# Optimization experiments

Measured on AMD Instinct MI355X. Metric: run time of the kernel, lower is better.

Reference implementation:

```python
import jax, jax.numpy as jnp
import numpy as np

B, S, E = 8, 2048, 512

def setup_inputs() -> dict:
    key = jax.random.key(0)
    ks = jax.random.split(key, 7)
    Q = jax.random.normal(ks[0], (B, S, E), dtype=jnp.float32)
    K = jax.random.normal(ks[1], (B, S, E), dtype=jnp.float32)
    pad_mask = jax.random.randint(ks[2], (B, S, S), 0, 2).astype(bool)
    # torch nn.Linear weights are [out, in]; y = x @ W.T + b
    sc = 1.0 / np.sqrt(E)
    Wq = jax.random.uniform(ks[3], (E, E), jnp.float32, -sc, sc)
    Wk = jax.random.uniform(ks[4], (E, E), jnp.float32, -sc, sc)
    Wv = jax.random.uniform(ks[5], (E, E), jnp.float32, -sc, sc)
    Wp = jax.random.uniform(ks[6], (E, E), jnp.float32, -sc, sc)
    bp = jnp.zeros((E,), jnp.float32)
    return {"Q": Q, "K": K, "pad_mask": pad_mask, "Wq": Wq, "Wk": Wk, "Wv": Wv, "Wp": Wp, "bp": bp}

def reference(Q, K, pad_mask, Wq, Wk, Wv, Wp, bp):
    scale = E ** (-0.5)
    V = K  # V aliases K before projection, as in the original
    q = jnp.einsum('bse,fe->bsf', Q, Wq)   # q_map (no bias)
    k = jnp.einsum('bse,fe->bsf', K, Wk)   # k_map
    v = jnp.einsum('bse,fe->bsf', V, Wv)   # v_map
    scores = jnp.einsum('bqe,bke->bqk', q, k) * scale  # [B,S,S]
    scores = jnp.where(pad_mask, -1e9, scores)
    attn = jax.nn.softmax(scores, axis=-1)
    out = jnp.einsum('bqk,bke->bqe', attn, v)
    out = jnp.einsum('bse,fe->bsf', out, Wp) + bp       # proj
    return q + out  # residual uses projected Q (faithful to source)
```

## Files before the change

### kernel.cpp

```cpp
#include <hip/hip_runtime.h>
#include <hip/hip_bf16.h>

typedef short v8s __attribute__((ext_vector_type(8)));
typedef float v4f __attribute__((ext_vector_type(4)));

static constexpr int BB = 8, SS = 2048, EE = 512;

enum { EPI_BF16 = 0, EPI_SCALE = 1, EPI_FINAL = 2 };

struct EpiParams {
  float scale;
  const float* bias;
  const __hip_bfloat16* resid;
  int resid_ld;
};

static constexpr int SMEM_BYTES = 34816;

struct CastParams {
  const float* src[4];
  __hip_bfloat16* dst[4];
};

__global__ __launch_bounds__(256) void cast_weights(CastParams cp) {
  const int seg = blockIdx.x >> 7;
  const int b = blockIdx.x & 127;
  const float* x = cp.src[seg] + (unsigned long long)b * 2048;
  __hip_bfloat16* y = cp.dst[seg] + (unsigned long long)b * 2048;
  int i = threadIdx.x * 8;
  float4 f0 = ((const float4*)(x + i))[0];
  float4 f1 = ((const float4*)(x + i))[1];
  alignas(16) __hip_bfloat16 h[8];
  h[0] = __float2bfloat16(f0.x); h[1] = __float2bfloat16(f0.y);
  h[2] = __float2bfloat16(f0.z); h[3] = __float2bfloat16(f0.w);
  h[4] = __float2bfloat16(f1.x); h[5] = __float2bfloat16(f1.y);
  h[6] = __float2bfloat16(f1.z); h[7] = __float2bfloat16(f1.w);
  *(uint4*)(y + i) = *(uint4*)h;
}

__device__ __forceinline__ void stage_tile64(const __hip_bfloat16* __restrict__ G,
                                             int row0, int ld, int k0,
                                             __hip_bfloat16* lds, int wave, int lane) {
#pragma unroll
  for (int t = 0; t < 4; ++t) {
    const int p = (wave * 4 + t) * 64 + lane;
    const int row = p >> 3;
    const int g = (p & 7) ^ (row & 7);
    const __hip_bfloat16* src = G + (unsigned long long)(row0 + row) * ld + k0 + g * 8;
    __builtin_amdgcn_global_load_lds(
        (const __attribute__((address_space(1))) void*)src,
        (__attribute__((address_space(3))) void*)(lds + (wave * 4 + t) * 512),
        16, 0, 0);
  }
}

__device__ __forceinline__ void stage_tile64_f32(const float* __restrict__ G,
                                                 int row0, int ld, int k0,
                                                 __hip_bfloat16* lds, int tid) {
#pragma unroll
  for (int c = 0; c < 4; ++c) {
    const int p = c * 256 + tid;
    const int row = p >> 3;
    const int g = (p & 7) ^ (row & 7);
    const float* src = G + (unsigned long long)(row0 + row) * ld + k0 + g * 8;
    float4 f0 = ((const float4*)src)[0];
    float4 f1 = ((const float4*)src)[1];
    alignas(16) __hip_bfloat16 h[8];
    h[0] = __float2bfloat16(f0.x); h[1] = __float2bfloat16(f0.y);
    h[2] = __float2bfloat16(f0.z); h[3] = __float2bfloat16(f0.w);
    h[4] = __float2bfloat16(f1.x); h[5] = __float2bfloat16(f1.y);
    h[6] = __float2bfloat16(f1.z); h[7] = __float2bfloat16(f1.w);
    *(uint4*)&lds[p * 8] = *(uint4*)h;
  }
}

template <int EPI, bool AF32, bool BF32>
__device__ __forceinline__ void gemm_body(const void* Agv, const void* Bgv,
                                          void* Cg, int K, int lda, int ldb, int ldc,
                                          int m0, int n0, const EpiParams& ep,
                                          unsigned char* smem) {
  __hip_bfloat16* As = (__hip_bfloat16*)smem;
  __hip_bfloat16* Bs = As + 128 * 64;

  const int tid = threadIdx.x;
  const int lane = tid & 63;
  const int wave = tid >> 6;
  const int wr = wave >> 1;
  const int wc = wave & 1;

  v4f acc[4][4];
  const v4f vzero = {0.f, 0.f, 0.f, 0.f};
#pragma unroll
  for (int i = 0; i < 4; ++i)
#pragma unroll
    for (int j = 0; j < 4; ++j) acc[i][j] = vzero;

  const int fr = lane & 15;
  const int fq = lane >> 4;

  for (int k0 = 0; k0 < K; k0 += 64) {
    __syncthreads();
    if constexpr (AF32)
      stage_tile64_f32((const float*)Agv, m0, lda, k0, As, tid);
    else
      stage_tile64((const __hip_bfloat16*)Agv, m0, lda, k0, As, wave, lane);
    if constexpr (BF32)
      stage_tile64_f32((const float*)Bgv, n0, ldb, k0, Bs, tid);
    else
      stage_tile64((const __hip_bfloat16*)Bgv, n0, ldb, k0, Bs, wave, lane);
    __syncthreads();

#pragma unroll
    for (int ks = 0; ks < 2; ++ks) {
      const int gq = ks * 4 + fq;
      v8s a[4], b[4];
#pragma unroll
      for (int i = 0; i < 4; ++i) {
        const int r = wr * 64 + i * 16 + fr;
        a[i] = *(const v8s*)&As[r * 64 + ((gq ^ (r & 7)) * 8)];
      }
#pragma unroll
      for (int j = 0; j < 4; ++j) {
        const int r = wc * 64 + j * 16 + fr;
        b[j] = *(const v8s*)&Bs[r * 64 + ((gq ^ (r & 7)) * 8)];
      }
#pragma unroll
      for (int i = 0; i < 4; ++i)
#pragma unroll
        for (int j = 0; j < 4; ++j)
          acc[i][j] = __builtin_amdgcn_mfma_f32_16x16x32_bf16(a[i], b[j], acc[i][j], 0, 0, 0);
    }
  }

  const int cf = lane & 15;
  const int rq = (lane >> 4) * 4;

  __syncthreads();

  if constexpr (EPI != EPI_FINAL) {
    __hip_bfloat16* Ct = (__hip_bfloat16*)smem;
    const int ST = 136;
#pragma unroll
    for (int i = 0; i < 4; ++i) {
      const int rl = wr * 64 + i * 16 + rq;
#pragma unroll
      for (int j = 0; j < 4; ++j) {
        const int col = wc * 64 + j * 16 + cf;
#pragma unroll
        for (int r = 0; r < 4; ++r) {
          float v = acc[i][j][r];
          if constexpr (EPI == EPI_SCALE) v *= ep.scale;
          Ct[(rl + r) * ST + col] = __float2bfloat16(v);
        }
      }
    }
    __syncthreads();
    __hip_bfloat16* C = (__hip_bfloat16*)Cg;
#pragma unroll
    for (int c = 0; c < 8; ++c) {
      const int idx = c * 256 + tid;
      const int row = idx >> 4;
      const int colc = (idx & 15) * 8;
      *(v8s*)&C[(unsigned long long)(m0 + row) * ldc + n0 + colc] =
          *(const v8s*)&Ct[row * ST + colc];
    }
  } else {
    float* Cf = (float*)smem;
    const int ST = 132;
    float* C = (float*)Cg;
#pragma unroll
    for (int h = 0; h < 2; ++h) {
      if (wr == h) {
#pragma unroll
        for (int i = 0; i < 4; ++i) {
          const int rl = i * 16 + rq;
#pragma unroll
          for (int j = 0; j < 4; ++j) {
            const int col = wc * 64 + j * 16 + cf;
#pragma unroll
            for (int r = 0; r < 4; ++r) Cf[(rl + r) * ST + col] = acc[i][j][r];
          }
        }
      }
      __syncthreads();
#pragma unroll
      for (int c = 0; c < 8; ++c) {
        const int idx = c * 256 + tid;
        const int row = idx >> 5;
        const int colc = (idx & 31) * 4;
        const int grow = m0 + h * 64 + row;
        const int gcol = n0 + colc;
        float4 v = *(const float4*)&Cf[row * ST + colc];
        float4 b4 = *(const float4*)&ep.bias[gcol];
        ushort4 r4 = *(const ushort4*)&ep.resid[(unsigned long long)grow * ep.resid_ld + gcol];
        v.x += b4.x + __bfloat162float(*(__hip_bfloat16*)&r4.x);
        v.y += b4.y + __bfloat162float(*(__hip_bfloat16*)&r4.y);
        v.z += b4.z + __bfloat162float(*(__hip_bfloat16*)&r4.z);
        v.w += b4.w + __bfloat162float(*(__hip_bfloat16*)&r4.w);
        *(float4*)&C[(unsigned long long)grow * ldc + gcol] = v;
      }
      if (h == 0) __syncthreads();
    }
  }
}

template <int EPI>
__global__ __launch_bounds__(256, 3) void gemm_bt(
    const __hip_bfloat16* __restrict__ Ag, const __hip_bfloat16* __restrict__ Bg,
    void* __restrict__ Cg, int K, int lda, int ldb, int ldc,
    unsigned long long sAz, unsigned long long sBz, unsigned long long sCz, EpiParams ep) {
  __shared__ __align__(16) unsigned char smem[SMEM_BYTES];
  const unsigned long long z = blockIdx.z;
  void* Cz;
  if constexpr (EPI == EPI_FINAL) Cz = (void*)((float*)Cg + z * sCz);
  else Cz = (void*)((__hip_bfloat16*)Cg + z * sCz);
  gemm_body<EPI, false, false>(Ag + z * sAz, Bg + z * sBz, Cz, K, lda, ldb, ldc,
                               blockIdx.y * 128, blockIdx.x * 128, ep, smem);
}

__global__ __launch_bounds__(256, 3) void gemm_qkv(
    const float* __restrict__ Q, const float* __restrict__ K,
    const __hip_bfloat16* __restrict__ Wq, const __hip_bfloat16* __restrict__ Wk,
    const __hip_bfloat16* __restrict__ Wv,
    __hip_bfloat16* __restrict__ qb, __hip_bfloat16* __restrict__ kb,
    __hip_bfloat16* __restrict__ vT) {
  __shared__ __align__(16) unsigned char smem[SMEM_BYTES];
  const int z = blockIdx.z;
  EpiParams ep{};
  if (z == 2) {
    gemm_body<EPI_BF16, false, true>(Wv, K, vT, EE, EE, EE, BB * SS,
                                     blockIdx.y * 128, blockIdx.x * 128, ep, smem);
  } else {
    const float* A = (z == 0) ? Q : K;
    const __hip_bfloat16* B = (z == 0) ? Wq : Wk;
    __hip_bfloat16* C = (z == 0) ? qb : kb;
    gemm_body<EPI_BF16, true, false>(A, B, C, EE, EE, EE, EE,
                                     blockIdx.x * 128, blockIdx.y * 128, ep, smem);
  }
}

static constexpr int FLASH_LDS = 149248;

__device__ __forceinline__ void stage_K64(const __hip_bfloat16* __restrict__ Kb, int kv0,
                                          __hip_bfloat16* lds, int tid) {
  const int wv = tid >> 6;
#pragma unroll
  for (int c = 0; c < 8; ++c) {
    const int p = c * 512 + tid;
    const int chunk = p >> 9;
    const int row = (p >> 3) & 63;
    const int g = (p & 7) ^ (row & 7);
    const __hip_bfloat16* src = Kb + (unsigned long long)(kv0 + row) * 512ull + chunk * 64 + g * 8;
    __builtin_amdgcn_global_load_lds(
        (const __attribute__((address_space(1))) void*)src,
        (__attribute__((address_space(3))) void*)(lds + (c * 512 + wv * 64) * 8),
        16, 0, 0);
  }
}

__device__ __forceinline__ void stage_mask(const unsigned char* __restrict__ Mb, int kv0,
                                           unsigned char* lds, int tid) {
  if (tid < 256) {
    const int row = tid >> 2;
    const int g = tid & 3;
    const unsigned char* src = Mb + (unsigned long long)row * 2048ull + kv0 + g * 16;
    __builtin_amdgcn_global_load_lds(
        (const __attribute__((address_space(1))) void*)src,
        (__attribute__((address_space(3))) void*)(lds + tid * 16),
        16, 0, 0);
  }
}

__global__ __launch_bounds__(512, 2) void flash_attn(
    const __hip_bfloat16* __restrict__ qb, const __hip_bfloat16* __restrict__ kb,
    const __hip_bfloat16* __restrict__ vT, const unsigned char* __restrict__ mask,
    __hip_bfloat16* __restrict__ ob) {
  extern __shared__ __align__(16) char fsm[];
  __hip_bfloat16* Ks0 = (__hip_bfloat16*)fsm;
  __hip_bfloat16* Ps  = (__hip_bfloat16*)(fsm + 131072);
  unsigned char* Msk  = (unsigned char*)(fsm + 139264);
  float* m_s  = (float*)(fsm + 147456);
  float* l_s  = (float*)(fsm + 147968);
  float* pmax = (float*)(fsm + 148224);
  float* psum = (float*)(fsm + 148736);

  const int tid = threadIdx.x;
  const int lane = tid & 63;
  const int w = tid >> 6;
  const int fr = lane & 15;
  const int fq = lane >> 4;
  const int wq = w & 3;
  const int wk = w >> 2;
  const int b = blockIdx.x & 7;
  const int q0 = (blockIdx.x >> 3) * 64;
  const unsigned long long bS = (unsigned long long)b * 2048ull;
  const float SC = 0.044194173824159216f;

  v8s qf[16];
  {
    const __hip_bfloat16* qrow = qb + (bS + q0 + wq * 16 + fr) * 512ull;
#pragma unroll
    for (int kk = 0; kk < 16; ++kk) qf[kk] = *(const v8s*)&qrow[kk * 32 + fq * 8];
  }

  v4f acc[4][4];
  const v4f vz = {0.f, 0.f, 0.f, 0.f};
#pragma unroll
  for (int i = 0; i < 4; ++i)
#pragma unroll
    for (int j = 0; j < 4; ++j) acc[i][j] = vz;

  if (tid < 64) { m_s[tid] = -1e30f; l_s[tid] = 0.f; }

  const __hip_bfloat16* Kb = kb + bS * 512ull;
  const unsigned char* Mb = mask + (bS + q0) * 2048ull;
  stage_K64(Kb, 0, Ks0, tid);
  stage_mask(Mb, 0, Msk, tid);
  __syncthreads();

  for (int t = 0; t < 32; ++t) {
    __hip_bfloat16* KsT = Ks0 + (t & 1) * 32768;
    const unsigned char* mskT = Msk + (t & 1) * 4096;
    const int kv0 = t * 64;

    if (t < 31) {
      stage_K64(Kb, (t + 1) * 64, Ks0 + ((t + 1) & 1) * 32768, tid);
      stage_mask(Mb, (t + 1) * 64, Msk + ((t + 1) & 1) * 4096, tid);
    }

    v8s vb[2][4];
#pragma unroll
    for (int ks = 0; ks < 2; ++ks)
#pragma unroll
      for (int j = 0; j < 4; ++j)
        vb[ks][j] = *(const v8s*)&vT[(unsigned long long)(w * 64 + j * 16 + fr) * 16384ull +
                                     bS + kv0 + ks * 32 + fq * 8];

    v4f sa[2] = {vz, vz};
    __builtin_amdgcn_s_setprio(1);
#pragma unroll
    for (int kk = 0; kk < 16; ++kk) {
#pragma unroll
      for (int j = 0; j < 2; ++j) {
        const int rr = wk * 32 + j * 16 + fr;
        v8s kf = *(const v8s*)&KsT[(kk >> 1) * 4096 + rr * 64 + ((((kk & 1) * 4 + fq) ^ (rr & 7)) * 8)];
        sa[j] = __builtin_amdgcn_mfma_f32_16x16x32_bf16(qf[kk], kf, sa[j], 0, 0, 0);
      }
    }
    __builtin_amdgcn_s_setprio(0);

    float sv[2][4];
    float rmx[4] = {-3e38f, -3e38f, -3e38f, -3e38f};
#pragma unroll
    for (int j = 0; j < 2; ++j) {
      const int col = wk * 32 + j * 16 + fr;
#pragma unroll
      for (int r = 0; r < 4; ++r) {
        const unsigned char mk = mskT[(wq * 16 + fq * 4 + r) * 64 + col];
        const float x = mk ? -1e9f : sa[j][r] * SC;
        sv[j][r] = x;
        rmx[r] = fmaxf(rmx[r], x);
      }
    }
#pragma unroll
    for (int off = 1; off <= 8; off <<= 1)
#pragma unroll
      for (int r = 0; r < 4; ++r) rmx[r] = fmaxf(rmx[r], __shfl_xor(rmx[r], off));
    if (fr == 0)
      *(float4*)&pmax[wk * 64 + wq * 16 + fq * 4] = make_float4(rmx[0], rmx[1], rmx[2], rmx[3]);

    asm volatile("s_waitcnt lgkmcnt(0)" ::: "memory");
    __builtin_amdgcn_s_barrier();
    __builtin_amdgcn_sched_barrier(0);

    const float* mo_cur = m_s + (t & 1) * 64;
    float* mo_nxt = m_s + ((t + 1) & 1) * 64;
    float mnr[4];
#pragma unroll
    for (int i = 0; i < 4; ++i) {
      const int r0 = i * 16 + fq * 4;
      float4 mo4 = *(const float4*)&mo_cur[r0];
      float4 p04 = *(const float4*)&pmax[r0];
      float4 p14 = *(const float4*)&pmax[64 + r0];
      float mn[4], fc[4];
      mn[0] = fmaxf(mo4.x, fmaxf(p04.x, p14.x));
      mn[1] = fmaxf(mo4.y, fmaxf(p04.y, p14.y));
      mn[2] = fmaxf(mo4.z, fmaxf(p04.z, p14.z));
      mn[3] = fmaxf(mo4.w, fmaxf(p04.w, p14.w));
      fc[0] = __expf(mo4.x - mn[0]);
      fc[1] = __expf(mo4.y - mn[1]);
      fc[2] = __expf(mo4.z - mn[2]);
      fc[3] = __expf(mo4.w - mn[3]);
#pragma unroll
      for (int j = 0; j < 4; ++j)
#pragma unroll
        for (int r = 0; r < 4; ++r) acc[i][j][r] *= fc[r];
      if (i == wq) { mnr[0] = mn[0]; mnr[1] = mn[1]; mnr[2] = mn[2]; mnr[3] = mn[3]; }
      if (w == 0 && fr == 0)
        *(float4*)&mo_nxt[r0] = make_float4(mn[0], mn[1], mn[2], mn[3]);
    }

    float rsm[4] = {0.f, 0.f, 0.f, 0.f};
#pragma unroll
    for (int j = 0; j < 2; ++j) {
      const int col = wk * 32 + j * 16 + fr;
      const int cg = col >> 3, cl = col & 7;
#pragma unroll
      for (int r = 0; r < 4; ++r) {
        const float p = __expf(sv[j][r] - mnr[r]);
        rsm[r] += p;
        const int row = wq * 16 + fq * 4 + r;
        Ps[row * 64 + ((cg ^ (row & 7)) * 8) + cl] = __float2bfloat16(p);
      }
    }
#pragma unroll
    for (int off = 1; off <= 8; off <<= 1)
#pragma unroll
      for (int r = 0; r < 4; ++r) rsm[r] += __shfl_xor(rsm[r], off);
    if (fr == 0)
      *(float4*)&psum[wk * 64 + wq * 16 + fq * 4] = make_float4(rsm[0], rsm[1], rsm[2], rsm[3]);

    asm volatile("s_waitcnt lgkmcnt(0)" ::: "memory");
    __builtin_amdgcn_s_barrier();
    __builtin_amdgcn_sched_barrier(0);

    if (tid < 64) {
      const float mo = mo_cur[tid];
      const float mn = fmaxf(mo, fmaxf(pmax[tid], pmax[64 + tid]));
      l_s[tid] = l_s[tid] * __expf(mo - mn) + psum[tid] + psum[64 + tid];
    }

    __builtin_amdgcn_s_setprio(1);
#pragma unroll
    for (int ks = 0; ks < 2; ++ks) {
      v8s pa[4];
#pragma unroll
      for (int i = 0; i < 4; ++i) {
        const int row = i * 16 + fr;
        pa[i] = *(const v8s*)&Ps[row * 64 + (((ks * 4 + fq) ^ (row & 7)) * 8)];
      }
#pragma unroll
      for (int i = 0; i < 4; ++i)
#pragma unroll
        for (int j = 0; j < 4; ++j)
          acc[i][j] = __builtin_amdgcn_mfma_f32_16x16x32_bf16(pa[i], vb[ks][j], acc[i][j], 0, 0, 0);
    }
    __builtin_amdgcn_s_setprio(0);

    asm volatile("s_waitcnt vmcnt(0) lgkmcnt(0)" ::: "memory");
    __builtin_amdgcn_s_barrier();
    __builtin_amdgcn_sched_barrier(0);
  }

#pragma unroll
  for (int i = 0; i < 4; ++i) {
    const float4 l4 = *(const float4*)&l_s[i * 16 + fq * 4];
    const float inv[4] = {1.f / l4.x, 1.f / l4.y, 1.f / l4.z, 1.f / l4.w};
#pragma unroll
    for (int r = 0; r < 4; ++r) {
      __hip_bfloat16* orow = ob + (bS + q0 + i * 16 + fq * 4 + r) * 512ull + w * 64 + fr;
#pragma unroll
      for (int j = 0; j < 4; ++j)
        orow[j * 16] = __float2bfloat16(acc[i][j][r] * inv[r]);
    }
  }
}

extern "C" void kernel_launch(void* const* d_in, const int* in_sizes, int n_in,
                              void* d_out, int out_size, void* d_ws, size_t ws_size,
                              hipStream_t stream) {
  const float* Q = (const float*)d_in[0];
  const float* K = (const float*)d_in[1];
  const unsigned char* mask = (const unsigned char*)d_in[2];
  const float* Wq = (const float*)d_in[3];
  const float* Wk = (const float*)d_in[4];
  const float* Wv = (const float*)d_in[5];
  const float* Wp = (const float*)d_in[6];
  const float* bp = (const float*)d_in[7];
  float* out = (float*)d_out;

  char* ws = (char*)d_ws;
  const unsigned long long MB = 1024ull * 1024ull;
  __hip_bfloat16* qb = (__hip_bfloat16*)(ws + 0 * MB);
  __hip_bfloat16* kb = (__hip_bfloat16*)(ws + 16 * MB);
  __hip_bfloat16* vT = (__hip_bfloat16*)(ws + 32 * MB);
  __hip_bfloat16* Wqb = (__hip_bfloat16*)(ws + 48 * MB);
  __hip_bfloat16* Wkb = Wqb + 512 * 512;
  __hip_bfloat16* Wvb = Wkb + 512 * 512;
  __hip_bfloat16* Wpb = Wvb + 512 * 512;
  __hip_bfloat16* ob = (__hip_bfloat16*)(ws + 64 * MB);

  dim3 blk(256, 1, 1);

  CastParams cp;
  cp.src[0] = Wq; cp.dst[0] = Wqb;
  cp.src[1] = Wk; cp.dst[1] = Wkb;
  cp.src[2] = Wv; cp.dst[2] = Wvb;
  cp.src[3] = Wp; cp.dst[3] = Wpb;
  cast_weights<<<dim3(512, 1, 1), blk, 0, stream>>>(cp);

  gemm_qkv<<<dim3((BB * SS) / 128, EE / 128, 3), blk, 0, stream>>>(
      Q, K, Wqb, Wkb, Wvb, qb, kb, vT);

  static bool attr_done = false;
  if (!attr_done) {
    hipFuncSetAttribute((const void*)flash_attn,
                        hipFuncAttributeMaxDynamicSharedMemorySize, FLASH_LDS);
    attr_done = true;
  }
  flash_attn<<<dim3(256, 1, 1), dim3(512, 1, 1), FLASH_LDS, stream>>>(
      qb, kb, vT, mask, ob);

  EpiParams epf{};
  epf.bias = bp;
  epf.resid = qb;
  epf.resid_ld = EE;
  gemm_bt<EPI_FINAL><<<dim3(EE / 128, (BB * SS) / 128, 1), blk, 0, stream>>>(
      ob, Wpb, out, EE, EE, EE, EE, 0ull, 0ull, 0ull, epf);
}
```

Measured before the change: 428.3 us.

## Shrink flash-attention tiles to 32 queries by 32 keys with 4 waves

Restructures the attention kernel from 64-query blocks of 8 waves with 64-key tiles to 32-query blocks of 4 waves with 32-key tiles, doubling the grid to 512 blocks and cutting LDS to about 71KB. The mask is now read directly from global memory into registers instead of being staged through LDS, and the P tile uses a padded stride instead of an XOR swizzle. The aim is more resident blocks and better occupancy. In exchange K and V are reloaded twice as often per query, there are twice as many barriers, and each wave does less MFMA work between syncs.

```diff
diff --git a/kernel.cpp b/kernel.cpp
--- a/kernel.cpp
+++ b/kernel.cpp
@@ -239,60 +239,47 @@
   }
 }
 
-static constexpr int FLASH_LDS = 149248;
-
-__device__ __forceinline__ void stage_K64(const __hip_bfloat16* __restrict__ Kb, int kv0,
-                                          __hip_bfloat16* lds, int tid) {
-  const int wv = tid >> 6;
-#pragma unroll
-  for (int c = 0; c < 8; ++c) {
-    const int p = c * 512 + tid;
-    const int chunk = p >> 9;
-    const int row = (p >> 3) & 63;
-    const int g = (p & 7) ^ (row & 7);
+static constexpr int PST = 72;
+static constexpr int FLASH_LDS = 65536 + 4608 + 1024;
+
+__device__ __forceinline__ void stage_K32(const __hip_bfloat16* __restrict__ Kb, int kv0,
+                                          __hip_bfloat16* lds, int w, int lane) {
+#pragma unroll
+  for (int t = 0; t < 8; ++t) {
+    const int id = w * 8 + t;
+    const int chunk = id >> 2;
+    const int rowblk = id & 3;
+    const int row = rowblk * 8 + (lane >> 3);
+    const int g = (lane & 7) ^ (row & 7);
     const __hip_bfloat16* src = Kb + (unsigned long long)(kv0 + row) * 512ull + chunk * 64 + g * 8;
     __builtin_amdgcn_global_load_lds(
         (const __attribute__((address_space(1))) void*)src,
-        (__attribute__((address_space(3))) void*)(lds + (c * 512 + wv * 64) * 8),
+        (__attribute__((address_space(3))) void*)(lds + chunk * 2048 + rowblk * 512),
         16, 0, 0);
   }
 }
 
-__device__ __forceinline__ void stage_mask(const unsigned char* __restrict__ Mb, int kv0,
-                                           unsigned char* lds, int tid) {
-  if (tid < 256) {
-    const int row = tid >> 2;
-    const int g = tid & 3;
-    const unsigned char* src = Mb + (unsigned long long)row * 2048ull + kv0 + g * 16;
-    __builtin_amdgcn_global_load_lds(
-        (const __attribute__((address_space(1))) void*)src,
-        (__attribute__((address_space(3))) void*)(lds + tid * 16),
-        16, 0, 0);
-  }
-}
-
-__global__ __launch_bounds__(512, 2) void flash_attn(
+__global__ __launch_bounds__(256, 2) void flash_attn(
     const __hip_bfloat16* __restrict__ qb, const __hip_bfloat16* __restrict__ kb,
     const __hip_bfloat16* __restrict__ vT, const unsigned char* __restrict__ mask,
     __hip_bfloat16* __restrict__ ob) {
   extern __shared__ __align__(16) char fsm[];
   __hip_bfloat16* Ks0 = (__hip_bfloat16*)fsm;
-  __hip_bfloat16* Ps  = (__hip_bfloat16*)(fsm + 131072);
-  unsigned char* Msk  = (unsigned char*)(fsm + 139264);
-  float* m_s  = (float*)(fsm + 147456);
-  float* l_s  = (float*)(fsm + 147968);
-  float* pmax = (float*)(fsm + 148224);
-  float* psum = (float*)(fsm + 148736);
+  __hip_bfloat16* Ps  = (__hip_bfloat16*)(fsm + 65536);
+  float* m_s  = (float*)(fsm + 65536 + 4608);
+  float* pmax = m_s + 64;
+  float* psum = pmax + 64;
+  float* l_s  = psum + 64;
 
   const int tid = threadIdx.x;
   const int lane = tid & 63;
   const int w = tid >> 6;
   const int fr = lane & 15;
   const int fq = lane >> 4;
-  const int wq = w & 3;
-  const int wk = w >> 2;
+  const int wq = w & 1;
+  const int wk = w >> 1;
   const int b = blockIdx.x & 7;
-  const int q0 = (blockIdx.x >> 3) * 64;
+  const int q0 = (blockIdx.x >> 3) * 32;
   const unsigned long long bS = (unsigned long long)b * 2048ull;
   const float SC = 0.044194173824159216f;
 
@@ -303,85 +290,74 @@
     for (int kk = 0; kk < 16; ++kk) qf[kk] = *(const v8s*)&qrow[kk * 32 + fq * 8];
   }
 
-  v4f acc[4][4];
+  v4f acc[2][8];
   const v4f vz = {0.f, 0.f, 0.f, 0.f};
 #pragma unroll
-  for (int i = 0; i < 4; ++i)
-#pragma unroll
-    for (int j = 0; j < 4; ++j) acc[i][j] = vz;
-
-  if (tid < 64) { m_s[tid] = -1e30f; l_s[tid] = 0.f; }
+  for (int i = 0; i < 2; ++i)
+#pragma unroll
+    for (int j = 0; j < 8; ++j) acc[i][j] = vz;
+
+  if (tid < 32) { m_s[tid] = -1e30f; l_s[tid] = 0.f; }
 
   const __hip_bfloat16* Kb = kb + bS * 512ull;
   const unsigned char* Mb = mask + (bS + q0) * 2048ull;
-  stage_K64(Kb, 0, Ks0, tid);
-  stage_mask(Mb, 0, Msk, tid);
+  stage_K32(Kb, 0, Ks0, w, lane);
   __syncthreads();
 
-  for (int t = 0; t < 32; ++t) {
-    __hip_bfloat16* KsT = Ks0 + (t & 1) * 32768;
-    const unsigned char* mskT = Msk + (t & 1) * 4096;
-    const int kv0 = t * 64;
-
-    if (t < 31) {
-      stage_K64(Kb, (t + 1) * 64, Ks0 + ((t + 1) & 1) * 32768, tid);
-      stage_mask(Mb, (t + 1) * 64, Msk + ((t + 1) & 1) * 4096, tid);
-    }
-
-    v8s vb[2][4];
-#pragma unroll
-    for (int ks = 0; ks < 2; ++ks)
-#pragma unroll
-      for (int j = 0; j < 4; ++j)
-        vb[ks][j] = *(const v8s*)&vT[(unsigned long long)(w * 64 + j * 16 + fr) * 16384ull +
-                                     bS + kv0 + ks * 32 + fq * 8];
-
-    v4f sa[2] = {vz, vz};
+  for (int t = 0; t < 64; ++t) {
+    __hip_bfloat16* KsT = Ks0 + (t & 1) * 16384;
+    const int kv0 = t * 32;
+
+    if (t < 63) stage_K32(Kb, (t + 1) * 32, Ks0 + ((t + 1) & 1) * 16384, w, lane);
+
+    unsigned char mk[4];
+#pragma unroll
+    for (int r = 0; r < 4; ++r)
+      mk[r] = Mb[(unsigned long long)(wq * 16 + fq * 4 + r) * 2048ull + kv0 + wk * 16 + fr];
+
+    v8s vb[8];
+#pragma unroll
+    for (int j = 0; j < 8; ++j)
+      vb[j] = *(const v8s*)&vT[(unsigned long long)(w * 128 + j * 16 + fr) * 16384ull +
+                               bS + kv0 + fq * 8];
+
+    v4f sa = vz;
     __builtin_amdgcn_s_setprio(1);
 #pragma unroll
     for (int kk = 0; kk < 16; ++kk) {
-#pragma unroll
-      for (int j = 0; j < 2; ++j) {
-        const int rr = wk * 32 + j * 16 + fr;
-        v8s kf = *(const v8s*)&KsT[(kk >> 1) * 4096 + rr * 64 + ((((kk & 1) * 4 + fq) ^ (rr & 7)) * 8)];
-        sa[j] = __builtin_amdgcn_mfma_f32_16x16x32_bf16(qf[kk], kf, sa[j], 0, 0, 0);
-      }
+      const int rr = wk * 16 + fr;
+      v8s kf = *(const v8s*)&KsT[(kk >> 1) * 2048 + rr * 64 + ((((kk & 1) * 4 + fq) ^ (rr & 7)) * 8)];
+      sa = __builtin_amdgcn_mfma_f32_16x16x32_bf16(qf[kk], kf, sa, 0, 0, 0);
     }
     __builtin_amdgcn_s_setprio(0);
 
-    float sv[2][4];
-    float rmx[4] = {-3e38f, -3e38f, -3e38f, -3e38f};
-#pragma unroll
-    for (int j = 0; j < 2; ++j) {
-      const int col = wk * 32 + j * 16 + fr;
-#pragma unroll
-      for (int r = 0; r < 4; ++r) {
-        const unsigned char mk = mskT[(wq * 16 + fq * 4 + r) * 64 + col];
-        const float x = mk ? -1e9f : sa[j][r] * SC;
-        sv[j][r] = x;
-        rmx[r] = fmaxf(rmx[r], x);
-      }
+    float sv[4];
+    float rmx[4];
+#pragma unroll
+    for (int r = 0; r < 4; ++r) {
+      sv[r] = mk[r] ? -1e9f : sa[r] * SC;
+      rmx[r] = sv[r];
     }
 #pragma unroll
     for (int off = 1; off <= 8; off <<= 1)
 #pragma unroll
       for (int r = 0; r < 4; ++r) rmx[r] = fmaxf(rmx[r], __shfl_xor(rmx[r], off));
     if (fr == 0)
-      *(float4*)&pmax[wk * 64 + wq * 16 + fq * 4] = make_float4(rmx[0], rmx[1], rmx[2], rmx[3]);
+      *(float4*)&pmax[wk * 32 + wq * 16 + fq * 4] = make_float4(rmx[0], rmx[1], rmx[2], rmx[3]);
 
     asm volatile("s_waitcnt lgkmcnt(0)" ::: "memory");
     __builtin_amdgcn_s_barrier();
     __builtin_amdgcn_sched_barrier(0);
 
-    const float* mo_cur = m_s + (t & 1) * 64;
-    float* mo_nxt = m_s + ((t + 1) & 1) * 64;
+    const float* mo_cur = m_s + (t & 1) * 32;
+    float* mo_nxt = m_s + ((t + 1) & 1) * 32;
     float mnr[4];
 #pragma unroll
-    for (int i = 0; i < 4; ++i) {
+    for (int i = 0; i < 2; ++i) {
       const int r0 = i * 16 + fq * 4;
       float4 mo4 = *(const float4*)&mo_cur[r0];
       float4 p04 = *(const float4*)&pmax[r0];
-      float4 p14 = *(const float4*)&pmax[64 + r0];
+      float4 p14 = *(const float4*)&pmax[32 + r0];
       float mn[4], fc[4];
       mn[0] = fmaxf(mo4.x, fmaxf(p04.x, p14.x));
       mn[1] = fmaxf(mo4.y, fmaxf(p04.y, p14.y));
@@ -392,7 +368,7 @@
       fc[2] = __expf(mo4.z - mn[2]);
       fc[3] = __expf(mo4.w - mn[3]);
 #pragma unroll
-      for (int j = 0; j < 4; ++j)
+      for (int j = 0; j < 8; ++j)
 #pragma unroll
         for (int r = 0; r < 4; ++r) acc[i][j][r] *= fc[r];
       if (i == wq) { mnr[0] = mn[0]; mnr[1] = mn[1]; mnr[2] = mn[2]; mnr[3] = mn[3]; }
@@ -400,51 +376,40 @@
         *(float4*)&mo_nxt[r0] = make_float4(mn[0], mn[1], mn[2], mn[3]);
     }
 
-    float rsm[4] = {0.f, 0.f, 0.f, 0.f};
-#pragma unroll
-    for (int j = 0; j < 2; ++j) {
-      const int col = wk * 32 + j * 16 + fr;
-      const int cg = col >> 3, cl = col & 7;
-#pragma unroll
-      for (int r = 0; r < 4; ++r) {
-        const float p = __expf(sv[j][r] - mnr[r]);
-        rsm[r] += p;
-        const int row = wq * 16 + fq * 4 + r;
-        Ps[row * 64 + ((cg ^ (row & 7)) * 8) + cl] = __float2bfloat16(p);
-      }
+    float rsm[4];
+#pragma unroll
+    for (int r = 0; r < 4; ++r) {
+      const float p = __expf(sv[r] - mnr[r]);
+      rsm[r] = p;
+      Ps[(wq * 16 + fq * 4 + r) * PST + wk * 16 + fr] = __float2bfloat16(p);
     }
 #pragma unroll
     for (int off = 1; off <= 8; off <<= 1)
 #pragma unroll
       for (int r = 0; r < 4; ++r) rsm[r] += __shfl_xor(rsm[r], off);
     if (fr == 0)
-      *(float4*)&psum[wk * 64 + wq * 16 + fq * 4] = make_float4(rsm[0], rsm[1], rsm[2], rsm[3]);
+      *(float4*)&psum[wk * 32 + wq * 16 + fq * 4] = make_float4(rsm[0], rsm[1], rsm[2], rsm[3]);
 
     asm volatile("s_waitcnt lgkmcnt(0)" ::: "memory");
     __builtin_amdgcn_s_barrier();
     __builtin_amdgcn_sched_barrier(0);
 
-    if (tid < 64) {
+    if (tid < 32) {
       const float mo = mo_cur[tid];
-      const float mn = fmaxf(mo, fmaxf(pmax[tid], pmax[64 + tid]));
-      l_s[tid] = l_s[tid] * __expf(mo - mn) + psum[tid] + psum[64 + tid];
+      const float mn = fmaxf(mo, fmaxf(pmax[tid], pmax[32 + tid]));
+      l_s[tid] = l_s[tid] * __expf(mo - mn) + psum[tid] + psum[32 + tid];
     }
 
     __builtin_amdgcn_s_setprio(1);
-#pragma unroll
-    for (int ks = 0; ks < 2; ++ks) {
-      v8s pa[4];
-#pragma unroll
-      for (int i = 0; i < 4; ++i) {
-        const int row = i * 16 + fr;
-        pa[i] = *(const v8s*)&Ps[row * 64 + (((ks * 4 + fq) ^ (row & 7)) * 8)];
-      }
-#pragma unroll
-      for (int i = 0; i < 4; ++i)
-#pragma unroll
-        for (int j = 0; j < 4; ++j)
-          acc[i][j] = __builtin_amdgcn_mfma_f32_16x16x32_bf16(pa[i], vb[ks][j], acc[i][j], 0, 0, 0);
-    }
+    v8s pa[2];
+#pragma unroll
+    for (int i = 0; i < 2; ++i)
+      pa[i] = *(const v8s*)&Ps[(i * 16 + fr) * PST + fq * 8];
+#pragma unroll
+    for (int i = 0; i < 2; ++i)
+#pragma unroll
+      for (int j = 0; j < 8; ++j)
+        acc[i][j] = __builtin_amdgcn_mfma_f32_16x16x32_bf16(pa[i], vb[j], acc[i][j], 0, 0, 0);
     __builtin_amdgcn_s_setprio(0);
 
     asm volatile("s_waitcnt vmcnt(0) lgkmcnt(0)" ::: "memory");
@@ -453,14 +418,14 @@
   }
 
 #pragma unroll
-  for (int i = 0; i < 4; ++i) {
+  for (int i = 0; i < 2; ++i) {
     const float4 l4 = *(const float4*)&l_s[i * 16 + fq * 4];
     const float inv[4] = {1.f / l4.x, 1.f / l4.y, 1.f / l4.z, 1.f / l4.w};
 #pragma unroll
     for (int r = 0; r < 4; ++r) {
-      __hip_bfloat16* orow = ob + (bS + q0 + i * 16 + fq * 4 + r) * 512ull + w * 64 + fr;
-#pragma unroll
-      for (int j = 0; j < 4; ++j)
+      __hip_bfloat16* orow = ob + (bS + q0 + i * 16 + fq * 4 + r) * 512ull + w * 128 + fr;
+#pragma unroll
+      for (int j = 0; j < 8; ++j)
         orow[j * 16] = __float2bfloat16(acc[i][j][r] * inv[r]);
     }
   }
@@ -508,7 +473,7 @@
                         hipFuncAttributeMaxDynamicSharedMemorySize, FLASH_LDS);
     attr_done = true;
   }
-  flash_attn<<<dim3(256, 1, 1), dim3(512, 1, 1), FLASH_LDS, stream>>>(
+  flash_attn<<<dim3(512, 1, 1), dim3(256, 1, 1), FLASH_LDS, stream>>>(
       qb, kb, vT, mask, ob);
 
   EpiParams epf{};
```

After: 449.7 us. 5.0% more time.
